# Kernel tuning notes

Measured on AMD Instinct MI355X. Metric: run time of the kernel, lower is better.

## Reference

```python
import jax, jax.numpy as jnp
import numpy as np

# CaMoE_Block MoE dispatch/combine reference.
# Assumptions (undefined submodules in source): RWKV7_TimeMix/att residual omitted
# (h = ln2(x) directly); SparseRWKVFFN experts modeled as RWKV channel-mix FFNs
# y = relu(h @ W1)^2 @ W2; the LinearTransformerExpert (last expert) uses the same
# FFN form with recon_loss = 0; per-expert confidence head conf_e = sigmoid(h @ wc_e + bc_e).
# Faithful parts: winner selection, winning-bid lookup, straight-through scale
# factor conf / (stop_grad(conf) + 1e-6), per-expert compute, scatter-combine, residual.

B, T, C = 4, 2048, 1024
E = 5            # num_rwkv_experts + 1
H = 4 * C        # FFN hidden
LN_EPS = 1e-5


def setup_inputs() -> dict:
    key = jax.random.key(0)
    ks = jax.random.split(key, 8)
    x = jax.random.normal(ks[0], (B, T, C), dtype=jnp.float32)
    winners = jax.random.randint(ks[1], (B, T), 0, E)
    gamma = jnp.ones((C,), jnp.float32)
    beta = jnp.zeros((C,), jnp.float32)
    w1 = jax.random.normal(ks[2], (E, C, H), jnp.float32) * (1.0 / np.sqrt(C))
    w2 = jax.random.normal(ks[3], (E, H, C), jnp.float32) * (1.0 / np.sqrt(H))
    wc = jax.random.normal(ks[4], (E, C), jnp.float32) * (1.0 / np.sqrt(C))
    bc = jnp.zeros((E,), jnp.float32)
    return {"x": x, "winners": winners, "gamma": gamma, "beta": beta,
            "w1": w1, "w2": w2, "wc": wc, "bc": bc}


def _layernorm(x, gamma, beta):
    mu = jnp.mean(x, axis=-1, keepdims=True)
    var = jnp.mean(jnp.square(x - mu), axis=-1, keepdims=True)
    return (x - mu) * jax.lax.rsqrt(var + LN_EPS) * gamma + beta


def reference(x, winners, gamma, beta, w1, w2, wc, bc):
    b, t, c = x.shape
    e = w1.shape[0]
    h = _layernorm(x, gamma, beta)
    hf = h.reshape(-1, c)                     # [N, C]
    win = winners.reshape(-1)                 # [N]

    # per-expert confidences (bids)
    conf = jax.nn.sigmoid(hf @ wc.T + bc)     # [N, E]
    winning_bids = jnp.take_along_axis(conf, win[:, None], axis=1)  # [N, 1]
    scale = winning_bids / (jax.lax.stop_gradient(winning_bids) + 1e-6)

    # dense all-expert FFN (squared-ReLU channel mix), then top-1 select
    k = jnp.square(jax.nn.relu(jnp.einsum('nc,ech->enh', hf, w1)))  # [E, N, H]
    y = jnp.einsum('enh,ehc->enc', k, w2)                            # [E, N, C]
    sel = jax.nn.one_hot(win, e, dtype=y.dtype)                      # [N, E]
    expert_out = jnp.einsum('ne,enc->nc', sel, y)                    # scatter-combine

    out = (expert_out * scale).reshape(b, t, c)
    return x + out
```

## Files before the change

kernel.cpp:

```cpp
#include <hip/hip_runtime.h>
#include <hip/hip_bf16.h>
#include <stdint.h>

#define N_TOK 8192
#define C_DIM 1024
#define H_DIM 4096
#define E_NUM 5
#define LN_EPS 1e-5f

typedef __hip_bfloat16 bf16;
using s8v = __attribute__((ext_vector_type(8))) short;
using f4v = __attribute__((ext_vector_type(4))) float;

__device__ __forceinline__ void async_ld16(const bf16* g, bf16* l) {
    __builtin_amdgcn_global_load_lds(
        (const __attribute__((address_space(1))) void*)g,
        (__attribute__((address_space(3))) void*)l,
        16, 0, 0);
}

__global__ void init_meta_kernel(int* meta) {
    if (threadIdx.x < 16) meta[threadIdx.x] = 0;
}

__global__ __launch_bounds__(256) void count_kernel(
    const int* __restrict__ win, int* __restrict__ meta)
{
    __shared__ int c[E_NUM];
    if (threadIdx.x < E_NUM) c[threadIdx.x] = 0;
    __syncthreads();
    int n = blockIdx.x * 256 + threadIdx.x;
    atomicAdd(&c[win[n]], 1);
    __syncthreads();
    if (threadIdx.x < E_NUM) atomicAdd(&meta[threadIdx.x], c[threadIdx.x]);
}

__global__ void scan_kernel(int* meta) {
    if (threadIdx.x == 0) {
        int off = 0;
        for (int e = 0; e < E_NUM; ++e) {
            meta[5 + e] = off;
            off += meta[e];
            meta[11 + e] = 0;
        }
        meta[5 + E_NUM] = off;
    }
}

__global__ __launch_bounds__(256) void scatter_kernel(
    const int* __restrict__ win, int* __restrict__ meta,
    int* __restrict__ idx, int* __restrict__ pos)
{
    __shared__ int c[E_NUM];
    __shared__ int base[E_NUM];
    if (threadIdx.x < E_NUM) c[threadIdx.x] = 0;
    __syncthreads();
    int n = blockIdx.x * 256 + threadIdx.x;
    int e = win[n];
    int lr = atomicAdd(&c[e], 1);
    __syncthreads();
    if (threadIdx.x < E_NUM)
        base[threadIdx.x] = atomicAdd(&meta[11 + threadIdx.x], c[threadIdx.x]);
    __syncthreads();
    int p = meta[5 + e] + base[e] + lr;
    idx[p] = n;
    pos[n] = p;
}

__global__ __launch_bounds__(256) void ln_conf_kernel(
    const float* __restrict__ x, const int* __restrict__ win,
    const float* __restrict__ gamma, const float* __restrict__ beta,
    const float* __restrict__ wc, const float* __restrict__ bc,
    const int* __restrict__ pos,
    bf16* __restrict__ hbuf, float* __restrict__ scl)
{
    int n = blockIdx.x;
    int t = threadIdx.x;
    const float* xr = x + (size_t)n * C_DIM;
    float v[4];
    float s = 0.f, ss = 0.f;
#pragma unroll
    for (int i = 0; i < 4; ++i) {
        v[i] = xr[t + i * 256];
        s += v[i];
        ss += v[i] * v[i];
    }
#pragma unroll
    for (int off = 32; off > 0; off >>= 1) {
        s  += __shfl_down(s, off);
        ss += __shfl_down(ss, off);
    }
    __shared__ float red[8];
    __shared__ float mu_s, rv_s;
    int wave = t >> 6, lane = t & 63;
    if (lane == 0) { red[wave] = s; red[4 + wave] = ss; }
    __syncthreads();
    if (t == 0) {
        float S  = red[0] + red[1] + red[2] + red[3];
        float SS = red[4] + red[5] + red[6] + red[7];
        float mu = S * (1.f / C_DIM);
        float var = SS * (1.f / C_DIM) - mu * mu;
        mu_s = mu;
        rv_s = rsqrtf(var + LN_EPS);
    }
    __syncthreads();
    float mu = mu_s, rv = rv_s;
    int e = win[n];
    int p = pos[n];
    const float* wce = wc + (size_t)e * C_DIM;
    float dot = 0.f;
#pragma unroll
    for (int i = 0; i < 4; ++i) {
        int ci = t + i * 256;
        float hv = (v[i] - mu) * rv * gamma[ci] + beta[ci];
        hbuf[(size_t)p * C_DIM + ci] = (bf16)hv;
        dot += hv * wce[ci];
    }
#pragma unroll
    for (int off = 32; off > 0; off >>= 1) dot += __shfl_down(dot, off);
    if (lane == 0) red[wave] = dot;
    __syncthreads();
    if (t == 0) {
        float z = red[0] + red[1] + red[2] + red[3] + bc[e];
        float conf = 1.f / (1.f + expf(-z));
        scl[p] = conf / (conf + 1e-6f);
    }
}

__global__ __launch_bounds__(256) void transpose_cvt_kernel(
    const float* __restrict__ src, bf16* __restrict__ dst, int R, int S)
{
    __shared__ float tile[64][65];
    size_t ebase = (size_t)blockIdx.z * (size_t)R * (size_t)S;
    int s0 = blockIdx.x * 64;
    int r0 = blockIdx.y * 64;
    int t = threadIdx.x;
    int lr = t >> 4;
    int lc = (t & 15) * 4;
#pragma unroll
    for (int i = 0; i < 4; ++i) {
        int r = lr + i * 16;
        float4 v = *(const float4*)(src + ebase + (size_t)(r0 + r) * S + s0 + lc);
        tile[r][lc + 0] = v.x;
        tile[r][lc + 1] = v.y;
        tile[r][lc + 2] = v.z;
        tile[r][lc + 3] = v.w;
    }
    __syncthreads();
    int sc = t >> 2;
#pragma unroll
    for (int p = 0; p < 2; ++p) {
        int ch = (t & 3) + p * 4;
        bf16 vals[8];
#pragma unroll
        for (int j = 0; j < 8; ++j)
            vals[j] = (bf16)tile[ch * 8 + j][sc];
        *(s8v*)(dst + ebase + (size_t)(s0 + sc) * R + r0 + ch * 8) = *(s8v*)vals;
    }
}


__global__ __launch_bounds__(256) void gemm1_kernel(
    const bf16* __restrict__ hbuf, const bf16* __restrict__ w1t,
    const int* __restrict__ meta, bf16* __restrict__ ks)
{
    int e = blockIdx.z;
    int base_p = meta[5 + e];
    int cnt = meta[6 + e] - base_p;
    int m0 = blockIdx.y * 128;
    if (m0 >= cnt) return;
    int n0 = blockIdx.x * 128;

    __shared__ __align__(16) bf16 As[128 * 32];
    __shared__ __align__(16) bf16 Bs[128 * 32];

    int t = threadIdx.x;
    int lane = t & 63;
    int wv = t >> 6;
    int wr = wv >> 1, wcol = wv & 1;

    int rowA = t >> 2;
    int kcol = (((t & 3) ^ (rowA & 3)) * 8);

    int r1 = min(m0 + rowA, cnt - 1);
    int r2 = min(m0 + 64 + rowA, cnt - 1);
    const bf16* ga1 = hbuf + (size_t)(base_p + r1) * C_DIM + kcol;
    const bf16* ga2 = hbuf + (size_t)(base_p + r2) * C_DIM + kcol;
    const bf16* wbase = w1t + (size_t)e * H_DIM * C_DIM;
    const bf16* gb1 = wbase + (size_t)(n0 + rowA) * C_DIM + kcol;
    const bf16* gb2 = wbase + (size_t)(n0 + 64 + rowA) * C_DIM + kcol;

    bf16* la1 = As + t * 8;
    bf16* la2 = As + 2048 + t * 8;
    bf16* lb1 = Bs + t * 8;
    bf16* lb2 = Bs + 2048 + t * 8;

    int koff = (((lane >> 4) ^ (lane & 3)) * 8);
    int arow = wr * 64 + (lane & 15);
    int brow = wcol * 64 + (lane & 15);

    f4v acc[4][4];
    f4v zero = {0.f, 0.f, 0.f, 0.f};
#pragma unroll
    for (int i = 0; i < 4; ++i)
#pragma unroll
        for (int j = 0; j < 4; ++j) acc[i][j] = zero;

    for (int kb = 0; kb < C_DIM / 32; ++kb) {
        __syncthreads();
        async_ld16(ga1, la1); ga1 += 32;
        async_ld16(ga2, la2); ga2 += 32;
        async_ld16(gb1, lb1); gb1 += 32;
        async_ld16(gb2, lb2); gb2 += 32;
        __syncthreads();
        s8v af[4], bfv[4];
#pragma unroll
        for (int mi = 0; mi < 4; ++mi)
            af[mi] = *(const s8v*)&As[(arow + mi * 16) * 32 + koff];
#pragma unroll
        for (int ni = 0; ni < 4; ++ni)
            bfv[ni] = *(const s8v*)&Bs[(brow + ni * 16) * 32 + koff];
#pragma unroll
        for (int mi = 0; mi < 4; ++mi)
#pragma unroll
            for (int ni = 0; ni < 4; ++ni)
                acc[mi][ni] = __builtin_amdgcn_mfma_f32_16x16x32_bf16(af[mi], bfv[ni], acc[mi][ni], 0, 0, 0);
    }

#pragma unroll
    for (int mi = 0; mi < 4; ++mi) {
#pragma unroll
        for (int r = 0; r < 4; ++r) {
            int row_local = wr * 64 + mi * 16 + ((lane >> 4) << 2) + r;
            int gm = m0 + row_local;
            if (gm < cnt) {
                size_t p = (size_t)(base_p + gm);
#pragma unroll
                for (int ni = 0; ni < 4; ++ni) {
                    int col = n0 + wcol * 64 + ni * 16 + (lane & 15);
                    float v = acc[mi][ni][r];
                    float rl = fmaxf(v, 0.f);
                    ks[p * H_DIM + col] = (bf16)(rl * rl);
                }
            }
        }
    }
}

__global__ __launch_bounds__(256) void gemm2_kernel(
    const bf16* __restrict__ ks, const bf16* __restrict__ w2t,
    const int* __restrict__ idx, const int* __restrict__ meta,
    const float* __restrict__ x, const float* __restrict__ scl,
    float* __restrict__ out)
{
    int e = blockIdx.z;
    int base_p = meta[5 + e];
    int cnt = meta[6 + e] - base_p;
    int m0 = blockIdx.y * 128;
    if (m0 >= cnt) return;
    int n0 = blockIdx.x * 128;

    __shared__ __align__(16) bf16 As[128 * 32];
    __shared__ __align__(16) bf16 Bs[128 * 32];

    int t = threadIdx.x;
    int lane = t & 63;
    int wv = t >> 6;
    int wr = wv >> 1, wcol = wv & 1;

    int rowA = t >> 2;
    int kcol = (((t & 3) ^ (rowA & 3)) * 8);

    int r1 = min(m0 + rowA, cnt - 1);
    int r2 = min(m0 + 64 + rowA, cnt - 1);
    const bf16* ga1 = ks + (size_t)(base_p + r1) * H_DIM + kcol;
    const bf16* ga2 = ks + (size_t)(base_p + r2) * H_DIM + kcol;
    const bf16* wbase = w2t + (size_t)e * C_DIM * H_DIM;
    const bf16* gb1 = wbase + (size_t)(n0 + rowA) * H_DIM + kcol;
    const bf16* gb2 = wbase + (size_t)(n0 + 64 + rowA) * H_DIM + kcol;

    bf16* la1 = As + t * 8;
    bf16* la2 = As + 2048 + t * 8;
    bf16* lb1 = Bs + t * 8;
    bf16* lb2 = Bs + 2048 + t * 8;

    int koff = (((lane >> 4) ^ (lane & 3)) * 8);
    int arow = wr * 64 + (lane & 15);
    int brow = wcol * 64 + (lane & 15);

    f4v acc[4][4];
    f4v zero = {0.f, 0.f, 0.f, 0.f};
#pragma unroll
    for (int i = 0; i < 4; ++i)
#pragma unroll
        for (int j = 0; j < 4; ++j) acc[i][j] = zero;

    for (int kb = 0; kb < H_DIM / 32; ++kb) {
        __syncthreads();
        async_ld16(ga1, la1); ga1 += 32;
        async_ld16(ga2, la2); ga2 += 32;
        async_ld16(gb1, lb1); gb1 += 32;
        async_ld16(gb2, lb2); gb2 += 32;
        __syncthreads();
        s8v af[4], bfv[4];
#pragma unroll
        for (int mi = 0; mi < 4; ++mi)
            af[mi] = *(const s8v*)&As[(arow + mi * 16) * 32 + koff];
#pragma unroll
        for (int ni = 0; ni < 4; ++ni)
            bfv[ni] = *(const s8v*)&Bs[(brow + ni * 16) * 32 + koff];
#pragma unroll
        for (int mi = 0; mi < 4; ++mi)
#pragma unroll
            for (int ni = 0; ni < 4; ++ni)
                acc[mi][ni] = __builtin_amdgcn_mfma_f32_16x16x32_bf16(af[mi], bfv[ni], acc[mi][ni], 0, 0, 0);
    }

#pragma unroll
    for (int mi = 0; mi < 4; ++mi) {
        int tok[4];
        float sclv[4];
#pragma unroll
        for (int r = 0; r < 4; ++r) {
            int row_local = wr * 64 + mi * 16 + ((lane >> 4) << 2) + r;
            int gm = m0 + row_local;
            if (gm < cnt) {
                tok[r] = idx[base_p + gm];
                sclv[r] = scl[base_p + gm];
            } else {
                tok[r] = -1;
                sclv[r] = 0.f;
            }
        }
#pragma unroll
        for (int ni = 0; ni < 4; ++ni) {
            int col = n0 + wcol * 64 + ni * 16 + (lane & 15);
#pragma unroll
            for (int r = 0; r < 4; ++r) {
                if (tok[r] >= 0) {
                    size_t o = (size_t)tok[r] * C_DIM + col;
                    out[o] = x[o] + acc[mi][ni][r] * sclv[r];
                }
            }
        }
    }
}

extern "C" void kernel_launch(void* const* d_in, const int* in_sizes, int n_in,
                              void* d_out, int out_size, void* d_ws, size_t ws_size,
                              hipStream_t stream) {
    const float* x     = (const float*)d_in[0];
    const int*   win   = (const int*)d_in[1];
    const float* gamma = (const float*)d_in[2];
    const float* beta  = (const float*)d_in[3];
    const float* w1    = (const float*)d_in[4];
    const float* w2    = (const float*)d_in[5];
    const float* wc    = (const float*)d_in[6];
    const float* bc    = (const float*)d_in[7];
    float* out = (float*)d_out;

    char* ws = (char*)d_ws;
    size_t o = 0;
    bf16* w1t  = (bf16*)(ws + o); o += (size_t)E_NUM * H_DIM * C_DIM * 2;
    bf16* w2t  = (bf16*)(ws + o); o += (size_t)E_NUM * C_DIM * H_DIM * 2;
    bf16* hbuf = (bf16*)(ws + o); o += (size_t)N_TOK * C_DIM * 2;
    bf16* ks   = (bf16*)(ws + o); o += (size_t)N_TOK * H_DIM * 2;
    float* scl = (float*)(ws + o); o += (size_t)N_TOK * 4;
    int* idx   = (int*)(ws + o);   o += (size_t)N_TOK * 4;
    int* pos   = (int*)(ws + o);   o += (size_t)N_TOK * 4;
    int* meta  = (int*)(ws + o);   o += 64;

    hipLaunchKernelGGL(init_meta_kernel, dim3(1), dim3(64), 0, stream, meta);
    hipLaunchKernelGGL(count_kernel, dim3(N_TOK / 256), dim3(256), 0, stream, win, meta);
    hipLaunchKernelGGL(scan_kernel, dim3(1), dim3(64), 0, stream, meta);
    hipLaunchKernelGGL(scatter_kernel, dim3(N_TOK / 256), dim3(256), 0, stream, win, meta, idx, pos);
    hipLaunchKernelGGL(transpose_cvt_kernel, dim3(H_DIM / 64, C_DIM / 64, E_NUM), dim3(256), 0, stream,
                       w1, w1t, C_DIM, H_DIM);
    hipLaunchKernelGGL(transpose_cvt_kernel, dim3(C_DIM / 64, H_DIM / 64, E_NUM), dim3(256), 0, stream,
                       w2, w2t, H_DIM, C_DIM);
    hipLaunchKernelGGL(ln_conf_kernel, dim3(N_TOK), dim3(256), 0, stream,
                       x, win, gamma, beta, wc, bc, pos, hbuf, scl);
    hipLaunchKernelGGL(gemm1_kernel, dim3(H_DIM / 128, 64, E_NUM), dim3(256), 0, stream,
                       hbuf, w1t, meta, ks);
    hipLaunchKernelGGL(gemm2_kernel, dim3(C_DIM / 128, 64, E_NUM), dim3(256), 0, stream,
                       ks, w2t, idx, meta, x, scl, out);
}
```

Baseline: 473.6 us.

## Double-buffer LDS tiles with K=64 steps in both expert GEMMs

Both grouped GEMM kernels move from a single K=32 LDS tile with two barriers per step to double-buffered K=64 tiles. The next tile is issued via global_load_lds while the current one feeds the MFMAs, with one barrier per iteration and an 8-way XOR swizzle for the wider rows. This aims to hide global load latency and halve barrier overhead. LDS use grows to 64KB per block, which may cut occupancy. The only barrier before reading the prefetched buffer sits after the compute, so correctness relies on that barrier also waiting for the async loads.

```diff
diff --git a/kernel.cpp b/kernel.cpp
--- a/kernel.cpp
+++ b/kernel.cpp
@@ -171,33 +171,30 @@
     if (m0 >= cnt) return;
     int n0 = blockIdx.x * 128;
 
-    __shared__ __align__(16) bf16 As[128 * 32];
-    __shared__ __align__(16) bf16 Bs[128 * 32];
+    __shared__ __align__(16) bf16 As[2][128 * 64];
+    __shared__ __align__(16) bf16 Bs[2][128 * 64];
 
     int t = threadIdx.x;
     int lane = t & 63;
     int wv = t >> 6;
     int wr = wv >> 1, wcol = wv & 1;
 
-    int rowA = t >> 2;
-    int kcol = (((t & 3) ^ (rowA & 3)) * 8);
-
-    int r1 = min(m0 + rowA, cnt - 1);
-    int r2 = min(m0 + 64 + rowA, cnt - 1);
-    const bf16* ga1 = hbuf + (size_t)(base_p + r1) * C_DIM + kcol;
-    const bf16* ga2 = hbuf + (size_t)(base_p + r2) * C_DIM + kcol;
+    const bf16* gA[4];
+    const bf16* gB[4];
     const bf16* wbase = w1t + (size_t)e * H_DIM * C_DIM;
-    const bf16* gb1 = wbase + (size_t)(n0 + rowA) * C_DIM + kcol;
-    const bf16* gb2 = wbase + (size_t)(n0 + 64 + rowA) * C_DIM + kcol;
-
-    bf16* la1 = As + t * 8;
-    bf16* la2 = As + 2048 + t * 8;
-    bf16* lb1 = Bs + t * 8;
-    bf16* lb2 = Bs + 2048 + t * 8;
-
-    int koff = (((lane >> 4) ^ (lane & 3)) * 8);
+#pragma unroll
+    for (int j = 0; j < 4; ++j) {
+        int chunk = j * 256 + t;
+        int row = chunk >> 3;
+        int gc = (chunk & 7) ^ (row & 7);
+        int ra = min(m0 + row, cnt - 1);
+        gA[j] = hbuf + (size_t)(base_p + ra) * C_DIM + gc * 8;
+        gB[j] = wbase + (size_t)(n0 + row) * C_DIM + gc * 8;
+    }
+
     int arow = wr * 64 + (lane & 15);
     int brow = wcol * 64 + (lane & 15);
+    int kq = lane >> 4;
 
     f4v acc[4][4];
     f4v zero = {0.f, 0.f, 0.f, 0.f};
@@ -206,25 +203,52 @@
 #pragma unroll
         for (int j = 0; j < 4; ++j) acc[i][j] = zero;
 
-    for (int kb = 0; kb < C_DIM / 32; ++kb) {
+    const int nk = C_DIM / 64;
+#pragma unroll
+    for (int j = 0; j < 4; ++j) {
+        async_ld16(gA[j], &As[0][(j * 256 + t) * 8]);
+        async_ld16(gB[j], &Bs[0][(j * 256 + t) * 8]);
+        gA[j] += 64;
+        gB[j] += 64;
+    }
+    __syncthreads();
+
+    int cur = 0;
+#pragma unroll 2
+    for (int kb = 0; kb < nk; ++kb) {
+        if (kb + 1 < nk) {
+            int nxt = cur ^ 1;
+#pragma unroll
+            for (int j = 0; j < 4; ++j) {
+                async_ld16(gA[j], &As[nxt][(j * 256 + t) * 8]);
+                async_ld16(gB[j], &Bs[nxt][(j * 256 + t) * 8]);
+                gA[j] += 64;
+                gB[j] += 64;
+            }
+        }
+#pragma unroll
+        for (int kk = 0; kk < 2; ++kk) {
+            s8v af[4], bfv[4];
+#pragma unroll
+            for (int mi = 0; mi < 4; ++mi) {
+                int r = arow + mi * 16;
+                int pc = (kk * 4 + kq) ^ (r & 7);
+                af[mi] = *(const s8v*)&As[cur][r * 64 + pc * 8];
+            }
+#pragma unroll
+            for (int ni = 0; ni < 4; ++ni) {
+                int r = brow + ni * 16;
+                int pc = (kk * 4 + kq) ^ (r & 7);
+                bfv[ni] = *(const s8v*)&Bs[cur][r * 64 + pc * 8];
+            }
+#pragma unroll
+            for (int mi = 0; mi < 4; ++mi)
+#pragma unroll
+                for (int ni = 0; ni < 4; ++ni)
+                    acc[mi][ni] = __builtin_amdgcn_mfma_f32_16x16x32_bf16(af[mi], bfv[ni], acc[mi][ni], 0, 0, 0);
+        }
         __syncthreads();
-        async_ld16(ga1, la1); ga1 += 32;
-        async_ld16(ga2, la2); ga2 += 32;
-        async_ld16(gb1, lb1); gb1 += 32;
-        async_ld16(gb2, lb2); gb2 += 32;
-        __syncthreads();
-        s8v af[4], bfv[4];
-#pragma unroll
-        for (int mi = 0; mi < 4; ++mi)
-            af[mi] = *(const s8v*)&As[(arow + mi * 16) * 32 + koff];
-#pragma unroll
-        for (int ni = 0; ni < 4; ++ni)
-            bfv[ni] = *(const s8v*)&Bs[(brow + ni * 16) * 32 + koff];
-#pragma unroll
-        for (int mi = 0; mi < 4; ++mi)
-#pragma unroll
-            for (int ni = 0; ni < 4; ++ni)
-                acc[mi][ni] = __builtin_amdgcn_mfma_f32_16x16x32_bf16(af[mi], bfv[ni], acc[mi][ni], 0, 0, 0);
+        cur ^= 1;
     }
 
 #pragma unroll
@@ -260,33 +284,30 @@
     if (m0 >= cnt) return;
     int n0 = blockIdx.x * 128;
 
-    __shared__ __align__(16) bf16 As[128 * 32];
-    __shared__ __align__(16) bf16 Bs[128 * 32];
+    __shared__ __align__(16) bf16 As[2][128 * 64];
+    __shared__ __align__(16) bf16 Bs[2][128 * 64];
 
     int t = threadIdx.x;
     int lane = t & 63;
     int wv = t >> 6;
     int wr = wv >> 1, wcol = wv & 1;
 
-    int rowA = t >> 2;
-    int kcol = (((t & 3) ^ (rowA & 3)) * 8);
-
-    int r1 = min(m0 + rowA, cnt - 1);
-    int r2 = min(m0 + 64 + rowA, cnt - 1);
-    const bf16* ga1 = ks + (size_t)(base_p + r1) * H_DIM + kcol;
-    const bf16* ga2 = ks + (size_t)(base_p + r2) * H_DIM + kcol;
+    const bf16* gA[4];
+    const bf16* gB[4];
     const bf16* wbase = w2t + (size_t)e * C_DIM * H_DIM;
-    const bf16* gb1 = wbase + (size_t)(n0 + rowA) * H_DIM + kcol;
-    const bf16* gb2 = wbase + (size_t)(n0 + 64 + rowA) * H_DIM + kcol;
-
-    bf16* la1 = As + t * 8;
-    bf16* la2 = As + 2048 + t * 8;
-    bf16* lb1 = Bs + t * 8;
-    bf16* lb2 = Bs + 2048 + t * 8;
-
-    int koff = (((lane >> 4) ^ (lane & 3)) * 8);
+#pragma unroll
+    for (int j = 0; j < 4; ++j) {
+        int chunk = j * 256 + t;
+        int row = chunk >> 3;
+        int gc = (chunk & 7) ^ (row & 7);
+        int ra = min(m0 + row, cnt - 1);
+        gA[j] = ks + (size_t)(base_p + ra) * H_DIM + gc * 8;
+        gB[j] = wbase + (size_t)(n0 + row) * H_DIM + gc * 8;
+    }
+
     int arow = wr * 64 + (lane & 15);
     int brow = wcol * 64 + (lane & 15);
+    int kq = lane >> 4;
 
     f4v acc[4][4];
     f4v zero = {0.f, 0.f, 0.f, 0.f};
@@ -295,25 +316,52 @@
 #pragma unroll
         for (int j = 0; j < 4; ++j) acc[i][j] = zero;
 
-    for (int kb = 0; kb < H_DIM / 32; ++kb) {
+    const int nk = H_DIM / 64;
+#pragma unroll
+    for (int j = 0; j < 4; ++j) {
+        async_ld16(gA[j], &As[0][(j * 256 + t) * 8]);
+        async_ld16(gB[j], &Bs[0][(j * 256 + t) * 8]);
+        gA[j] += 64;
+        gB[j] += 64;
+    }
+    __syncthreads();
+
+    int cur = 0;
+#pragma unroll 2
+    for (int kb = 0; kb < nk; ++kb) {
+        if (kb + 1 < nk) {
+            int nxt = cur ^ 1;
+#pragma unroll
+            for (int j = 0; j < 4; ++j) {
+                async_ld16(gA[j], &As[nxt][(j * 256 + t) * 8]);
+                async_ld16(gB[j], &Bs[nxt][(j * 256 + t) * 8]);
+                gA[j] += 64;
+                gB[j] += 64;
+            }
+        }
+#pragma unroll
+        for (int kk = 0; kk < 2; ++kk) {
+            s8v af[4], bfv[4];
+#pragma unroll
+            for (int mi = 0; mi < 4; ++mi) {
+                int r = arow + mi * 16;
+                int pc = (kk * 4 + kq) ^ (r & 7);
+                af[mi] = *(const s8v*)&As[cur][r * 64 + pc * 8];
+            }
+#pragma unroll
+            for (int ni = 0; ni < 4; ++ni) {
+                int r = brow + ni * 16;
+                int pc = (kk * 4 + kq) ^ (r & 7);
+                bfv[ni] = *(const s8v*)&Bs[cur][r * 64 + pc * 8];
+            }
+#pragma unroll
+            for (int mi = 0; mi < 4; ++mi)
+#pragma unroll
+                for (int ni = 0; ni < 4; ++ni)
+                    acc[mi][ni] = __builtin_amdgcn_mfma_f32_16x16x32_bf16(af[mi], bfv[ni], acc[mi][ni], 0, 0, 0);
+        }
         __syncthreads();
-        async_ld16(ga1, la1); ga1 += 32;
-        async_ld16(ga2, la2); ga2 += 32;
-        async_ld16(gb1, lb1); gb1 += 32;
-        async_ld16(gb2, lb2); gb2 += 32;
-        __syncthreads();
-        s8v af[4], bfv[4];
-#pragma unroll
-        for (int mi = 0; mi < 4; ++mi)
-            af[mi] = *(const s8v*)&As[(arow + mi * 16) * 32 + koff];
-#pragma unroll
-        for (int ni = 0; ni < 4; ++ni)
-            bfv[ni] = *(const s8v*)&Bs[(brow + ni * 16) * 32 + koff];
-#pragma unroll
-        for (int mi = 0; mi < 4; ++mi)
-#pragma unroll
-            for (int ni = 0; ni < 4; ++ni)
-                acc[mi][ni] = __builtin_amdgcn_mfma_f32_16x16x32_bf16(af[mi], bfv[ni], acc[mi][ni], 0, 0, 0);
+        cur ^= 1;
     }
 
 #pragma unroll
```

Result: slower. 523.8 us (+10.6%).

## Split-K gemm2 with atomic accumulation and remap LDS tile layout for conflict-free fragment loads

Applied to the files above, without the earlier changes.

gemm2 now splits the H reduction in two halves across the grid z dimension and accumulates partial results into out with atomicAdd. The residual x is written into out by the LayerNorm kernel beforehand. This doubles the block count of the gemm2 grid, which had few blocks. Both GEMMs also get a new swizzled LDS staging layout, so each fragment read uses a fixed pointer plus a constant offset, meant to cut bank conflicts and address arithmetic. The cost is float atomics on out and nondeterministic summation order.

```diff
diff --git a/kernel.cpp b/kernel.cpp
--- a/kernel.cpp
+++ b/kernel.cpp
@@ -72,7 +72,8 @@
     const float* __restrict__ gamma, const float* __restrict__ beta,
     const float* __restrict__ wc, const float* __restrict__ bc,
     const int* __restrict__ pos,
-    bf16* __restrict__ hbuf, float* __restrict__ scl)
+    bf16* __restrict__ hbuf, float* __restrict__ scl,
+    float* __restrict__ out)
 {
     int n = blockIdx.x;
     int t = threadIdx.x;
@@ -114,6 +115,7 @@
         int ci = t + i * 256;
         float hv = (v[i] - mu) * rv * gamma[ci] + beta[ci];
         hbuf[(size_t)p * C_DIM + ci] = (bf16)hv;
+        out[(size_t)n * C_DIM + ci] = v[i];
         dot += hv * wce[ci];
     }
 #pragma unroll
@@ -179,25 +181,29 @@
     int wv = t >> 6;
     int wr = wv >> 1, wcol = wv & 1;
 
-    int rowA = t >> 2;
-    int kcol = (((t & 3) ^ (rowA & 3)) * 8);
-
-    int r1 = min(m0 + rowA, cnt - 1);
-    int r2 = min(m0 + 64 + rowA, cnt - 1);
-    const bf16* ga1 = hbuf + (size_t)(base_p + r1) * C_DIM + kcol;
-    const bf16* ga2 = hbuf + (size_t)(base_p + r2) * C_DIM + kcol;
+    int i0 = (t & 7) ^ ((t >> 3) & 7);
+    int srow = 2 * (t >> 3) + (i0 >> 2);
+    int schk = i0 & 3;
+
+    int r1 = min(m0 + srow, cnt - 1);
+    int r2 = min(m0 + 64 + srow, cnt - 1);
+    const bf16* ga1 = hbuf + (size_t)(base_p + r1) * C_DIM + schk * 8;
+    const bf16* ga2 = hbuf + (size_t)(base_p + r2) * C_DIM + schk * 8;
     const bf16* wbase = w1t + (size_t)e * H_DIM * C_DIM;
-    const bf16* gb1 = wbase + (size_t)(n0 + rowA) * C_DIM + kcol;
-    const bf16* gb2 = wbase + (size_t)(n0 + 64 + rowA) * C_DIM + kcol;
+    const bf16* gb1 = wbase + (size_t)(n0 + srow) * C_DIM + schk * 8;
+    const bf16* gb2 = wbase + (size_t)(n0 + 64 + srow) * C_DIM + schk * 8;
 
     bf16* la1 = As + t * 8;
     bf16* la2 = As + 2048 + t * 8;
     bf16* lb1 = Bs + t * 8;
     bf16* lb2 = Bs + 2048 + t * 8;
 
-    int koff = (((lane >> 4) ^ (lane & 3)) * 8);
-    int arow = wr * 64 + (lane & 15);
-    int brow = wcol * 64 + (lane & 15);
+    int kq = lane >> 4;
+    int rhalf = (lane & 15) >> 1;
+    int ifrag = ((lane & 1) << 2) | kq;
+    int foff = rhalf * 64 + (ifrag ^ rhalf) * 8;
+    const bf16* Af = As + wr * 2048 + foff;
+    const bf16* Bf = Bs + wcol * 2048 + foff;
 
     f4v acc[4][4];
     f4v zero = {0.f, 0.f, 0.f, 0.f};
@@ -216,10 +222,10 @@
         s8v af[4], bfv[4];
 #pragma unroll
         for (int mi = 0; mi < 4; ++mi)
-            af[mi] = *(const s8v*)&As[(arow + mi * 16) * 32 + koff];
+            af[mi] = *(const s8v*)(Af + mi * 512);
 #pragma unroll
         for (int ni = 0; ni < 4; ++ni)
-            bfv[ni] = *(const s8v*)&Bs[(brow + ni * 16) * 32 + koff];
+            bfv[ni] = *(const s8v*)(Bf + ni * 512);
 #pragma unroll
         for (int mi = 0; mi < 4; ++mi)
 #pragma unroll
@@ -250,15 +256,17 @@
 __global__ __launch_bounds__(256) void gemm2_kernel(
     const bf16* __restrict__ ks, const bf16* __restrict__ w2t,
     const int* __restrict__ idx, const int* __restrict__ meta,
-    const float* __restrict__ x, const float* __restrict__ scl,
-    float* __restrict__ out)
-{
-    int e = blockIdx.z;
+    const float* __restrict__ scl, float* __restrict__ out)
+{
+    int z = blockIdx.z;
+    int e = z >> 1;
+    int kh = z & 1;
     int base_p = meta[5 + e];
     int cnt = meta[6 + e] - base_p;
     int m0 = blockIdx.y * 128;
     if (m0 >= cnt) return;
     int n0 = blockIdx.x * 128;
+    int kbase = kh * (H_DIM / 2);
 
     __shared__ __align__(16) bf16 As[128 * 32];
     __shared__ __align__(16) bf16 Bs[128 * 32];
@@ -268,25 +276,29 @@
     int wv = t >> 6;
     int wr = wv >> 1, wcol = wv & 1;
 
-    int rowA = t >> 2;
-    int kcol = (((t & 3) ^ (rowA & 3)) * 8);
-
-    int r1 = min(m0 + rowA, cnt - 1);
-    int r2 = min(m0 + 64 + rowA, cnt - 1);
-    const bf16* ga1 = ks + (size_t)(base_p + r1) * H_DIM + kcol;
-    const bf16* ga2 = ks + (size_t)(base_p + r2) * H_DIM + kcol;
+    int i0 = (t & 7) ^ ((t >> 3) & 7);
+    int srow = 2 * (t >> 3) + (i0 >> 2);
+    int schk = i0 & 3;
+
+    int r1 = min(m0 + srow, cnt - 1);
+    int r2 = min(m0 + 64 + srow, cnt - 1);
+    const bf16* ga1 = ks + (size_t)(base_p + r1) * H_DIM + kbase + schk * 8;
+    const bf16* ga2 = ks + (size_t)(base_p + r2) * H_DIM + kbase + schk * 8;
     const bf16* wbase = w2t + (size_t)e * C_DIM * H_DIM;
-    const bf16* gb1 = wbase + (size_t)(n0 + rowA) * H_DIM + kcol;
-    const bf16* gb2 = wbase + (size_t)(n0 + 64 + rowA) * H_DIM + kcol;
+    const bf16* gb1 = wbase + (size_t)(n0 + srow) * H_DIM + kbase + schk * 8;
+    const bf16* gb2 = wbase + (size_t)(n0 + 64 + srow) * H_DIM + kbase + schk * 8;
 
     bf16* la1 = As + t * 8;
     bf16* la2 = As + 2048 + t * 8;
     bf16* lb1 = Bs + t * 8;
     bf16* lb2 = Bs + 2048 + t * 8;
 
-    int koff = (((lane >> 4) ^ (lane & 3)) * 8);
-    int arow = wr * 64 + (lane & 15);
-    int brow = wcol * 64 + (lane & 15);
+    int kq = lane >> 4;
+    int rhalf = (lane & 15) >> 1;
+    int ifrag = ((lane & 1) << 2) | kq;
+    int foff = rhalf * 64 + (ifrag ^ rhalf) * 8;
+    const bf16* Af = As + wr * 2048 + foff;
+    const bf16* Bf = Bs + wcol * 2048 + foff;
 
     f4v acc[4][4];
     f4v zero = {0.f, 0.f, 0.f, 0.f};
@@ -295,7 +307,7 @@
 #pragma unroll
         for (int j = 0; j < 4; ++j) acc[i][j] = zero;
 
-    for (int kb = 0; kb < H_DIM / 32; ++kb) {
+    for (int kb = 0; kb < (H_DIM / 2) / 32; ++kb) {
         __syncthreads();
         async_ld16(ga1, la1); ga1 += 32;
         async_ld16(ga2, la2); ga2 += 32;
@@ -305,10 +317,10 @@
         s8v af[4], bfv[4];
 #pragma unroll
         for (int mi = 0; mi < 4; ++mi)
-            af[mi] = *(const s8v*)&As[(arow + mi * 16) * 32 + koff];
+            af[mi] = *(const s8v*)(Af + mi * 512);
 #pragma unroll
         for (int ni = 0; ni < 4; ++ni)
-            bfv[ni] = *(const s8v*)&Bs[(brow + ni * 16) * 32 + koff];
+            bfv[ni] = *(const s8v*)(Bf + ni * 512);
 #pragma unroll
         for (int mi = 0; mi < 4; ++mi)
 #pragma unroll
@@ -339,7 +351,7 @@
             for (int r = 0; r < 4; ++r) {
                 if (tok[r] >= 0) {
                     size_t o = (size_t)tok[r] * C_DIM + col;
-                    out[o] = x[o] + acc[mi][ni][r] * sclv[r];
+                    atomicAdd(&out[o], acc[mi][ni][r] * sclv[r]);
                 }
             }
         }
@@ -379,9 +391,9 @@
     hipLaunchKernelGGL(transpose_cvt_kernel, dim3(C_DIM / 64, H_DIM / 64, E_NUM), dim3(256), 0, stream,
                        w2, w2t, H_DIM, C_DIM);
     hipLaunchKernelGGL(ln_conf_kernel, dim3(N_TOK), dim3(256), 0, stream,
-                       x, win, gamma, beta, wc, bc, pos, hbuf, scl);
+                       x, win, gamma, beta, wc, bc, pos, hbuf, scl, out);
     hipLaunchKernelGGL(gemm1_kernel, dim3(H_DIM / 128, 64, E_NUM), dim3(256), 0, stream,
                        hbuf, w1t, meta, ks);
-    hipLaunchKernelGGL(gemm2_kernel, dim3(C_DIM / 128, 64, E_NUM), dim3(256), 0, stream,
-                       ks, w2t, idx, meta, x, scl, out);
-}
+    hipLaunchKernelGGL(gemm2_kernel, dim3(C_DIM / 128, 64, E_NUM * 2), dim3(256), 0, stream,
+                       ks, w2t, idx, meta, scl, out);
+}
```

Measured after the change: 504.6 us. +6.6%, slower.
